# Kernel optimization log

Measured on AMD Instinct MI355X. Metric: run time of the kernel, lower is better.

Reference implementation:

```python
import jax, jax.numpy as jnp
import numpy as np

D_MODEL = 1024
NHEAD = 16
D_K = D_MODEL // NHEAD


def setup_inputs() -> dict:
    key = jax.random.key(0)
    ks = jax.random.split(key, 11)
    B, S = 4, 2048
    s = 1.0 / np.sqrt(D_MODEL)
    return {
        "query": jax.random.normal(ks[0], (B, S, D_MODEL), jnp.float32),
        "key": jax.random.normal(ks[1], (B, S, D_MODEL), jnp.float32),
        "value": jax.random.normal(ks[2], (B, S, D_MODEL), jnp.float32),
        "Wq": jax.random.normal(ks[3], (D_MODEL, D_MODEL), jnp.float32) * s,
        "bq": jnp.zeros((D_MODEL,), jnp.float32),
        "Wk": jax.random.normal(ks[4], (D_MODEL, D_MODEL), jnp.float32) * s,
        "bk": jnp.zeros((D_MODEL,), jnp.float32),
        "Wv": jax.random.normal(ks[5], (D_MODEL, D_MODEL), jnp.float32) * s,
        "bv": jnp.zeros((D_MODEL,), jnp.float32),
        "Wo": jax.random.normal(ks[6], (D_MODEL, D_MODEL), jnp.float32) * s,
        "bo": jnp.zeros((D_MODEL,), jnp.float32),
    }


def _split_heads(x):
    # [B, S, D] -> [B, H, S, d_k]
    B, S, _ = x.shape
    return x.reshape(B, S, NHEAD, D_K).transpose(0, 2, 1, 3)


def reference(query, key, value, Wq, bq, Wk, bk, Wv, bv, Wo, bo):
    # torch Linear: x @ W.T + b
    q = _split_heads(query @ Wq.T + bq)
    k = _split_heads(key @ Wk.T + bk)
    v = _split_heads(value @ Wv.T + bv)
    scale = 1.0 / np.sqrt(D_K).astype(np.float32)
    scores = jnp.einsum("bhqd,bhkd->bhqk", q, k) * scale
    attn = jax.nn.softmax(scores, axis=-1)  # dropout p=0 -> identity
    out = jnp.einsum("bhqk,bhkd->bhqd", attn, v)
    B, H, S, dk = out.shape
    out = out.transpose(0, 2, 1, 3).reshape(B, S, H * dk)
    return out @ Wo.T + bo
```

## Files before the change

kernel.cpp:

```cpp
#include <hip/hip_runtime.h>
#include <stdint.h>

#define DEVI static __device__ __forceinline__

typedef __attribute__((ext_vector_type(4))) float f32x4;
typedef __attribute__((ext_vector_type(16))) float f32x16;
typedef __attribute__((ext_vector_type(8))) __bf16 bf16x8;
typedef __attribute__((ext_vector_type(4))) uint16_t u16x4;
typedef uint16_t u16;

DEVI u16 f2bf(float f) {
  union { float f; uint32_t u; } v; v.f = f;
  uint32_t r = v.u + 0x7FFFu + ((v.u >> 16) & 1u);
  return (u16)(r >> 16);
}

DEVI f32x4 mfma16(bf16x8 a, bf16x8 b, f32x4 c) {
  return __builtin_amdgcn_mfma_f32_16x16x32_bf16(a, b, c, 0, 0, 0);
}

DEVI f32x16 mfma32(bf16x8 a, bf16x8 b, f32x16 c) {
  return __builtin_amdgcn_mfma_f32_32x32x16_bf16(a, b, c, 0, 0, 0);
}

DEVI void load_lds16(const void* g, void* l) {
  __builtin_amdgcn_global_load_lds(
      (const __attribute__((address_space(1))) void*)g,
      (__attribute__((address_space(3))) void*)l, 16, 0, 0);
}

DEVI bf16x8 lds_frag(const u16* p) { return *(const bf16x8*)p; }

DEVI f32x16 zero16() {
  f32x16 z;
#pragma unroll
  for (int i = 0; i < 16; ++i) z[i] = 0.f;
  return z;
}

DEVI float exp2_hw(float x) {
  float r;
  asm("v_exp_f32 %0, %1" : "=v"(r) : "v"(x));
  return r;
}

DEVI uint32_t cvtpk(float lo, float hi) {
  uint32_t r;
  asm("v_cvt_pk_bf16_f32 %0, %1, %2" : "=v"(r) : "v"(lo), "v"(hi));
  return r;
}

DEVI float partner_f(float x) { return __shfl_xor(x, 32, 64); }

DEVI void pswap_asm(uint32_t& a, uint32_t& b) {
  asm("v_permlane32_swap_b32 %0, %1" : "+v"(a), "+v"(b));
}

#define NBIG (4 * 2048 * 1024)
#define NW (1024 * 1024)

__global__ __launch_bounds__(256) void cvt_kernel(
    const float* q, const float* k, const float* v, const float* Wq,
    const float* Wk, const float* Wv, const float* Wo, u16* qb, u16* kb,
    u16* vb, u16* Wqb, u16* Wkb, u16* Wvb, u16* Wob) {
  const float* src;
  u16* dst;
  int n;
  switch (blockIdx.y) {
    case 0: src = q;  dst = qb;  n = NBIG; break;
    case 1: src = k;  dst = kb;  n = NBIG; break;
    case 2: src = v;  dst = vb;  n = NBIG; break;
    case 3: src = Wq; dst = Wqb; n = NW;   break;
    case 4: src = Wk; dst = Wkb; n = NW;   break;
    case 5: src = Wv; dst = Wvb; n = NW;   break;
    default: src = Wo; dst = Wob; n = NW;  break;
  }
  int i = (blockIdx.x * 256 + threadIdx.x) * 4;
  if (i >= n) return;
  float4 f = *(const float4*)&src[i];
  u16x4 o;
  o.x = f2bf(f.x); o.y = f2bf(f.y); o.z = f2bf(f.z); o.w = f2bf(f.w);
  *(u16x4*)&dst[i] = o;
}

DEVI void gemm_core_1024(const u16* __restrict__ A, const u16* __restrict__ Bm,
                         int bm, int bn, u16* As, u16* Bs, f32x4 acc[4][4]) {
  const int tid = threadIdx.x;
  const int w = tid >> 6, l = tid & 63;
  const int lr = l & 15, lg = l >> 4;
  const int wr = (w >> 1) * 64, wc = (w & 1) * 64;

  for (int i = 0; i < 4; ++i)
    for (int j = 0; j < 4; ++j) acc[i][j] = (f32x4){0.f, 0.f, 0.f, 0.f};

  const int c0 = 2 * w, c1 = 2 * w + 1;
  const u16* gA0 = A + (size_t)(bm * 128 + c0 * 16 + (l >> 2)) * 1024 + (l & 3) * 8;
  const u16* gA1 = A + (size_t)(bm * 128 + c1 * 16 + (l >> 2)) * 1024 + (l & 3) * 8;
  const u16* gB0 = Bm + (size_t)(bn * 128 + c0 * 16 + (l >> 2)) * 1024 + (l & 3) * 8;
  const u16* gB1 = Bm + (size_t)(bn * 128 + c1 * 16 + (l >> 2)) * 1024 + (l & 3) * 8;
  u16* lA0 = As + c0 * 512;
  u16* lA1 = As + c1 * 512;
  u16* lB0 = Bs + c0 * 512;
  u16* lB1 = Bs + c1 * 512;

  int aoff[4], boff[4];
#pragma unroll
  for (int mi = 0; mi < 4; ++mi) aoff[mi] = (wr + mi * 16 + lr) * 32 + lg * 8;
#pragma unroll
  for (int nj = 0; nj < 4; ++nj) boff[nj] = (wc + nj * 16 + lr) * 32 + lg * 8;

  for (int k0 = 0; k0 < 1024; k0 += 32) {
    load_lds16(gA0 + k0, lA0);
    load_lds16(gA1 + k0, lA1);
    load_lds16(gB0 + k0, lB0);
    load_lds16(gB1 + k0, lB1);
    __syncthreads();
    bf16x8 af[4], bff[4];
#pragma unroll
    for (int mi = 0; mi < 4; ++mi) af[mi] = lds_frag(&As[aoff[mi]]);
#pragma unroll
    for (int nj = 0; nj < 4; ++nj) bff[nj] = lds_frag(&Bs[boff[nj]]);
#pragma unroll
    for (int mi = 0; mi < 4; ++mi)
#pragma unroll
      for (int nj = 0; nj < 4; ++nj)
        acc[mi][nj] = mfma16(af[mi], bff[nj], acc[mi][nj]);
    __syncthreads();
  }
}

__global__ __launch_bounds__(256) void proj_kernel(
    const u16* qb, const u16* kb, const u16* vb, const u16* Wq, const u16* Wk,
    const u16* Wv, const float* bq, const float* bk, const float* bv, u16* Qp,
    u16* Kp, u16* Vt) {
  __shared__ __align__(16) u16 As[128 * 32];
  __shared__ __align__(16) u16 Bs[128 * 32];
  const int z = blockIdx.z;
  const u16* A = z == 0 ? qb : z == 1 ? kb : vb;
  const u16* W = z == 0 ? Wq : z == 1 ? Wk : Wv;
  const float* bias = z == 0 ? bq : z == 1 ? bk : bv;

  f32x4 acc[4][4];
  gemm_core_1024(A, W, blockIdx.x, blockIdx.y, As, Bs, acc);

  const int tid = threadIdx.x;
  const int w = tid >> 6, l = tid & 63;
  const int lr = l & 15, lg = l >> 4;
  const int wr = (w >> 1) * 64, wc = (w & 1) * 64;
  const int b = (blockIdx.x * 128) >> 11;

#pragma unroll
  for (int nj = 0; nj < 4; ++nj) {
    const int col = blockIdx.y * 128 + wc + nj * 16 + lr;
    const float bb = bias[col];
    const int h = col >> 6, d = col & 63;
#pragma unroll
    for (int mi = 0; mi < 4; ++mi) {
      const int m0 = blockIdx.x * 128 + wr + mi * 16 + lg * 4;
      const int s0 = m0 & 2047;
      if (z < 2) {
        u16* dst = (z == 0) ? Qp : Kp;
#pragma unroll
        for (int r = 0; r < 4; ++r)
          dst[(((size_t)(b * 16 + h) * 2048) + s0 + r) * 64 + d] =
              f2bf(acc[mi][nj][r] + bb);
      } else {
        u16x4 pk;
        pk.x = f2bf(acc[mi][nj][0] + bb);
        pk.y = f2bf(acc[mi][nj][1] + bb);
        pk.z = f2bf(acc[mi][nj][2] + bb);
        pk.w = f2bf(acc[mi][nj][3] + bb);
        *(u16x4*)&Vt[(((size_t)(b * 16 + h) * 64) + d) * 2048 + s0] = pk;
      }
    }
  }
}

__global__ __launch_bounds__(256) void outproj_kernel(const u16* O,
                                                      const u16* Wo,
                                                      const float* bo,
                                                      float* out) {
  __shared__ __align__(16) u16 As[128 * 32];
  __shared__ __align__(16) u16 Bs[128 * 32];
  f32x4 acc[4][4];
  gemm_core_1024(O, Wo, blockIdx.x, blockIdx.y, As, Bs, acc);

  const int tid = threadIdx.x;
  const int w = tid >> 6, l = tid & 63;
  const int lr = l & 15, lg = l >> 4;
  const int wr = (w >> 1) * 64, wc = (w & 1) * 64;
#pragma unroll
  for (int nj = 0; nj < 4; ++nj) {
    const int col = blockIdx.y * 128 + wc + nj * 16 + lr;
    const float bb = bo[col];
#pragma unroll
    for (int mi = 0; mi < 4; ++mi) {
      const int m0 = blockIdx.x * 128 + wr + mi * 16 + lg * 4;
#pragma unroll
      for (int r = 0; r < 4; ++r)
        out[(size_t)(m0 + r) * 1024 + col] = acc[mi][nj][r] + bb;
    }
  }
}

#define LDPK 72
#define NT 32
__global__ __launch_bounds__(256) void attn_kernel(const u16* Qp, const u16* Kp,
                                                   const u16* Vt, u16* Ob) {
  __shared__ __align__(16) u16 Kl[2][64 * LDPK];
  __shared__ __align__(16) u16 Vl[2][64 * LDPK];

  const int tid = threadIdx.x, w = tid >> 6, l = tid & 63;
  const int q = l & 31, hi = l >> 5;
  const int bh = blockIdx.y;
  const int q0 = blockIdx.x * 128 + w * 32;
  const u16* Qh = Qp + (size_t)bh * 2048 * 64;
  const u16* Kh = Kp + (size_t)bh * 2048 * 64;
  const u16* Vh = Vt + (size_t)bh * 64 * 2048;

  const float SC2 = 0.1803368801f;

  bf16x8 qf[4];
#pragma unroll
  for (int ds = 0; ds < 4; ++ds)
    qf[ds] = *(const bf16x8*)&Qh[(size_t)(q0 + q) * 64 + ds * 16 + hi * 8];

  f32x16 o0 = zero16(), o1 = zero16();
  float m = -1.0e30f, ln = 0.f;

  const int r0 = tid >> 3, g0 = tid & 7;
  const int r1 = r0 + 32;

  int koff[2][4], voff[2][4];
#pragma unroll
  for (int kb = 0; kb < 2; ++kb)
#pragma unroll
    for (int ds = 0; ds < 4; ++ds)
      koff[kb][ds] = (kb * 32 + q) * LDPK + ds * 16 + hi * 8;
#pragma unroll
  for (int db = 0; db < 2; ++db)
#pragma unroll
    for (int ks = 0; ks < 4; ++ks)
      voff[db][ks] = (db * 32 + q) * LDPK + ks * 16 + hi * 8;

  bf16x8 kv0 = *(const bf16x8*)&Kh[r0 * 64 + g0 * 8];
  bf16x8 kv1 = *(const bf16x8*)&Kh[r1 * 64 + g0 * 8];
  bf16x8 vv0 = *(const bf16x8*)&Vh[(size_t)r0 * 2048 + g0 * 8];
  bf16x8 vv1 = *(const bf16x8*)&Vh[(size_t)r1 * 2048 + g0 * 8];
  *(bf16x8*)&Kl[0][r0 * LDPK + g0 * 8] = kv0;
  *(bf16x8*)&Kl[0][r1 * LDPK + g0 * 8] = kv1;
  *(bf16x8*)&Vl[0][r0 * LDPK + g0 * 8] = vv0;
  *(bf16x8*)&Vl[0][r1 * LDPK + g0 * 8] = vv1;
  kv0 = *(const bf16x8*)&Kh[4096 + r0 * 64 + g0 * 8];
  kv1 = *(const bf16x8*)&Kh[4096 + r1 * 64 + g0 * 8];
  vv0 = *(const bf16x8*)&Vh[(size_t)r0 * 2048 + 64 + g0 * 8];
  vv1 = *(const bf16x8*)&Vh[(size_t)r1 * 2048 + 64 + g0 * 8];
  const u16* gk0 = Kh + 2 * 4096 + r0 * 64 + g0 * 8;
  const u16* gk1 = Kh + 2 * 4096 + r1 * 64 + g0 * 8;
  const u16* gv0 = Vh + (size_t)r0 * 2048 + 2 * 64 + g0 * 8;
  const u16* gv1 = Vh + (size_t)r1 * 2048 + 2 * 64 + g0 * 8;
  __syncthreads();

  for (int kt = 0; kt < NT; ++kt) {
    const int cur = kt & 1;
    const u16* Kc = Kl[cur];
    const u16* Vc = Vl[cur];

    f32x16 c0 = zero16(), c1 = zero16();
    __builtin_amdgcn_s_setprio(1);
#pragma unroll
    for (int ds = 0; ds < 4; ++ds)
      c0 = mfma32(lds_frag(&Kc[koff[0][ds]]), qf[ds], c0);
#pragma unroll
    for (int ds = 0; ds < 4; ++ds)
      c1 = mfma32(lds_frag(&Kc[koff[1][ds]]), qf[ds], c1);
    __builtin_amdgcn_s_setprio(0);

    float tm[16];
#pragma unroll
    for (int r = 0; r < 16; ++r) tm[r] = fmaxf(c0[r], c1[r]);
#pragma unroll
    for (int s = 8; s > 0; s >>= 1)
#pragma unroll
      for (int r = 0; r < s; ++r) tm[r] = fmaxf(tm[r], tm[r + s]);
    const float mx = fmaxf(tm[0], partner_f(tm[0]));
    if (!__all(mx - m <= 64.0f)) {
      const float mnew = fmaxf(m, mx);
      const float a = exp2_hw((m - mnew) * SC2);
      m = mnew;
#pragma unroll
      for (int r = 0; r < 16; ++r) { o0[r] *= a; o1[r] *= a; }
      ln *= a;
    }
    const float m2 = m * SC2;
    float p0[16], p1[16];
#pragma unroll
    for (int r = 0; r < 16; ++r) {
      p0[r] = exp2_hw(__builtin_fmaf(c0[r], SC2, -m2));
      p1[r] = exp2_hw(__builtin_fmaf(c1[r], SC2, -m2));
    }
    float ts[16];
#pragma unroll
    for (int r = 0; r < 16; ++r) ts[r] = p0[r] + p1[r];
#pragma unroll
    for (int s = 8; s > 0; s >>= 1)
#pragma unroll
      for (int r = 0; r < s; ++r) ts[r] += ts[r + s];
    ln += ts[0] + partner_f(ts[0]);

    if (kt + 1 < NT) {
      u16* Kn = Kl[cur ^ 1];
      u16* Vn = Vl[cur ^ 1];
      *(bf16x8*)&Kn[r0 * LDPK + g0 * 8] = kv0;
      *(bf16x8*)&Kn[r1 * LDPK + g0 * 8] = kv1;
      *(bf16x8*)&Vn[r0 * LDPK + g0 * 8] = vv0;
      *(bf16x8*)&Vn[r1 * LDPK + g0 * 8] = vv1;
    }
    if (kt + 2 < NT) {
      kv0 = *(const bf16x8*)gk0;
      kv1 = *(const bf16x8*)gk1;
      vv0 = *(const bf16x8*)gv0;
      vv1 = *(const bf16x8*)gv1;
      gk0 += 4096; gk1 += 4096; gv0 += 64; gv1 += 64;
    }

    uint32_t wv[16];
#pragma unroll
    for (int i = 0; i < 8; ++i) {
      wv[i]     = cvtpk(p0[2 * i], p0[2 * i + 1]);
      wv[8 + i] = cvtpk(p1[2 * i], p1[2 * i + 1]);
    }
    bf16x8 pa[4];
#pragma unroll
    for (int ks = 0; ks < 4; ++ks) {
      const int base = (ks >> 1) * 8 + 4 * (ks & 1);
      uint32_t x0 = wv[base],     y0 = wv[base + 2];
      uint32_t x1 = wv[base + 1], y1 = wv[base + 3];
      pswap_asm(x0, y0);
      pswap_asm(x1, y1);
      union { uint32_t u[4]; bf16x8 v; } cvt;
      cvt.u[0] = x0; cvt.u[1] = x1; cvt.u[2] = y0; cvt.u[3] = y1;
      pa[ks] = cvt.v;
    }

    __builtin_amdgcn_s_setprio(1);
#pragma unroll
    for (int ks = 0; ks < 4; ++ks)
      o0 = mfma32(lds_frag(&Vc[voff[0][ks]]), pa[ks], o0);
#pragma unroll
    for (int ks = 0; ks < 4; ++ks)
      o1 = mfma32(lds_frag(&Vc[voff[1][ks]]), pa[ks], o1);
    __builtin_amdgcn_s_setprio(0);

    __syncthreads();
  }

  const int b2 = bh >> 4, h = bh & 15;
  const float inv = 1.0f / ln;
  u16* orow = Ob + ((size_t)(b2 * 2048 + q0 + q)) * 1024 + h * 64;
#pragma unroll
  for (int g = 0; g < 4; ++g) {
    u16x4 pk;
    pk.x = f2bf(o0[4 * g + 0] * inv);
    pk.y = f2bf(o0[4 * g + 1] * inv);
    pk.z = f2bf(o0[4 * g + 2] * inv);
    pk.w = f2bf(o0[4 * g + 3] * inv);
    *(u16x4*)&orow[8 * g + 4 * hi] = pk;
  }
#pragma unroll
  for (int g = 0; g < 4; ++g) {
    u16x4 pk;
    pk.x = f2bf(o1[4 * g + 0] * inv);
    pk.y = f2bf(o1[4 * g + 1] * inv);
    pk.z = f2bf(o1[4 * g + 2] * inv);
    pk.w = f2bf(o1[4 * g + 3] * inv);
    *(u16x4*)&orow[32 + 8 * g + 4 * hi] = pk;
  }
}

extern "C" void kernel_launch(void* const* d_in, const int* in_sizes, int n_in,
                              void* d_out, int out_size, void* d_ws,
                              size_t ws_size, hipStream_t stream) {
  const float* q  = (const float*)d_in[0];
  const float* k  = (const float*)d_in[1];
  const float* v  = (const float*)d_in[2];
  const float* Wq = (const float*)d_in[3];
  const float* bq = (const float*)d_in[4];
  const float* Wk = (const float*)d_in[5];
  const float* bk = (const float*)d_in[6];
  const float* Wv = (const float*)d_in[7];
  const float* bv = (const float*)d_in[8];
  const float* Wo = (const float*)d_in[9];
  const float* bo = (const float*)d_in[10];
  float* out = (float*)d_out;

  u16* ws = (u16*)d_ws;
  u16* qb  = ws;
  u16* kb  = qb + NBIG;
  u16* vb  = kb + NBIG;
  u16* Wqb = vb + NBIG;
  u16* Wkb = Wqb + NW;
  u16* Wvb = Wkb + NW;
  u16* Wob = Wvb + NW;
  u16* Qp  = Wob + NW;
  u16* Kp  = Qp + NBIG;
  u16* Vt  = Kp + NBIG;
  u16* O   = qb;

  cvt_kernel<<<dim3(8192, 7, 1), 256, 0, stream>>>(q, k, v, Wq, Wk, Wv, Wo, qb,
                                                   kb, vb, Wqb, Wkb, Wvb, Wob);
  proj_kernel<<<dim3(64, 8, 3), 256, 0, stream>>>(qb, kb, vb, Wqb, Wkb, Wvb,
                                                  bq, bk, bv, Qp, Kp, Vt);
  attn_kernel<<<dim3(16, 64, 1), 256, 0, stream>>>(Qp, Kp, Vt, O);
  outproj_kernel<<<dim3(64, 8, 1), 256, 0, stream>>>(O, Wob, bo, out);
}
```

Before: 235.6 us.

## Fuse fp32-to-bf16 activation conversion into projection GEMM A-tile loads

The separate conversion pass over the query, key and value activations is removed; the projection GEMM now reads fp32 rows directly, converts them to bf16 in registers, and writes them to LDS. The next k-step's A tile is register-prefetched so the conversion overlaps the MFMA work. The attention softmax row-max reduction also switches to v_max3 instructions. The goal is to avoid writing and re-reading about 48 MB of bf16 intermediates, at the cost of double the global A-read bytes per GEMM tile and more registers per thread.

```diff
diff --git a/kernel.cpp b/kernel.cpp
--- a/kernel.cpp
+++ b/kernel.cpp
@@ -50,33 +50,46 @@
   return r;
 }
 
+DEVI float max3f(float a, float b, float c) {
+  float r;
+  asm("v_max3_f32 %0, %1, %2, %3" : "=v"(r) : "v"(a), "v"(b), "v"(c));
+  return r;
+}
+
 DEVI float partner_f(float x) { return __shfl_xor(x, 32, 64); }
 
 DEVI void pswap_asm(uint32_t& a, uint32_t& b) {
   asm("v_permlane32_swap_b32 %0, %1" : "+v"(a), "+v"(b));
 }
 
+DEVI bf16x8 cvt8(float4 lo, float4 hi) {
+  union { uint32_t u[4]; bf16x8 v; } c;
+  c.u[0] = cvtpk(lo.x, lo.y);
+  c.u[1] = cvtpk(lo.z, lo.w);
+  c.u[2] = cvtpk(hi.x, hi.y);
+  c.u[3] = cvtpk(hi.z, hi.w);
+  return c.v;
+}
+
 #define NBIG (4 * 2048 * 1024)
 #define NW (1024 * 1024)
 
-__global__ __launch_bounds__(256) void cvt_kernel(
-    const float* q, const float* k, const float* v, const float* Wq,
-    const float* Wk, const float* Wv, const float* Wo, u16* qb, u16* kb,
-    u16* vb, u16* Wqb, u16* Wkb, u16* Wvb, u16* Wob) {
+__global__ __launch_bounds__(256) void cvt_kernel(const float* Wq,
+                                                  const float* Wk,
+                                                  const float* Wv,
+                                                  const float* Wo, u16* Wqb,
+                                                  u16* Wkb, u16* Wvb,
+                                                  u16* Wob) {
   const float* src;
   u16* dst;
-  int n;
   switch (blockIdx.y) {
-    case 0: src = q;  dst = qb;  n = NBIG; break;
-    case 1: src = k;  dst = kb;  n = NBIG; break;
-    case 2: src = v;  dst = vb;  n = NBIG; break;
-    case 3: src = Wq; dst = Wqb; n = NW;   break;
-    case 4: src = Wk; dst = Wkb; n = NW;   break;
-    case 5: src = Wv; dst = Wvb; n = NW;   break;
-    default: src = Wo; dst = Wob; n = NW;  break;
+    case 0: src = Wq; dst = Wqb; break;
+    case 1: src = Wk; dst = Wkb; break;
+    case 2: src = Wv; dst = Wvb; break;
+    default: src = Wo; dst = Wob; break;
   }
   int i = (blockIdx.x * 256 + threadIdx.x) * 4;
-  if (i >= n) return;
+  if (i >= NW) return;
   float4 f = *(const float4*)&src[i];
   u16x4 o;
   o.x = f2bf(f.x); o.y = f2bf(f.y); o.z = f2bf(f.z); o.w = f2bf(f.w);
@@ -129,19 +142,77 @@
   }
 }
 
+DEVI void gemm_core_f32A(const float* __restrict__ A32,
+                         const u16* __restrict__ Bm, int bm, int bn, u16* As,
+                         u16* Bs, f32x4 acc[4][4]) {
+  const int tid = threadIdx.x;
+  const int w = tid >> 6, l = tid & 63;
+  const int lr = l & 15, lg = l >> 4;
+  const int wr = (w >> 1) * 64, wc = (w & 1) * 64;
+
+  for (int i = 0; i < 4; ++i)
+    for (int j = 0; j < 4; ++j) acc[i][j] = (f32x4){0.f, 0.f, 0.f, 0.f};
+
+  const int c0 = 2 * w, c1 = 2 * w + 1;
+  const float* gA0 = A32 + (size_t)(bm * 128 + c0 * 16 + (l >> 2)) * 1024 + (l & 3) * 8;
+  const float* gA1 = A32 + (size_t)(bm * 128 + c1 * 16 + (l >> 2)) * 1024 + (l & 3) * 8;
+  const u16* gB0 = Bm + (size_t)(bn * 128 + c0 * 16 + (l >> 2)) * 1024 + (l & 3) * 8;
+  const u16* gB1 = Bm + (size_t)(bn * 128 + c1 * 16 + (l >> 2)) * 1024 + (l & 3) * 8;
+  u16* wA0 = As + c0 * 512 + l * 8;
+  u16* wA1 = As + c1 * 512 + l * 8;
+  u16* lB0 = Bs + c0 * 512;
+  u16* lB1 = Bs + c1 * 512;
+
+  int aoff[4], boff[4];
+#pragma unroll
+  for (int mi = 0; mi < 4; ++mi) aoff[mi] = (wr + mi * 16 + lr) * 32 + lg * 8;
+#pragma unroll
+  for (int nj = 0; nj < 4; ++nj) boff[nj] = (wc + nj * 16 + lr) * 32 + lg * 8;
+
+  float4 a0l = *(const float4*)(gA0);
+  float4 a0h = *(const float4*)(gA0 + 4);
+  float4 a1l = *(const float4*)(gA1);
+  float4 a1h = *(const float4*)(gA1 + 4);
+
+  for (int k0 = 0; k0 < 1024; k0 += 32) {
+    *(bf16x8*)wA0 = cvt8(a0l, a0h);
+    *(bf16x8*)wA1 = cvt8(a1l, a1h);
+    load_lds16(gB0 + k0, lB0);
+    load_lds16(gB1 + k0, lB1);
+    __syncthreads();
+    if (k0 + 32 < 1024) {
+      a0l = *(const float4*)(gA0 + k0 + 32);
+      a0h = *(const float4*)(gA0 + k0 + 36);
+      a1l = *(const float4*)(gA1 + k0 + 32);
+      a1h = *(const float4*)(gA1 + k0 + 36);
+    }
+    bf16x8 af[4], bff[4];
+#pragma unroll
+    for (int mi = 0; mi < 4; ++mi) af[mi] = lds_frag(&As[aoff[mi]]);
+#pragma unroll
+    for (int nj = 0; nj < 4; ++nj) bff[nj] = lds_frag(&Bs[boff[nj]]);
+#pragma unroll
+    for (int mi = 0; mi < 4; ++mi)
+#pragma unroll
+      for (int nj = 0; nj < 4; ++nj)
+        acc[mi][nj] = mfma16(af[mi], bff[nj], acc[mi][nj]);
+    __syncthreads();
+  }
+}
+
 __global__ __launch_bounds__(256) void proj_kernel(
-    const u16* qb, const u16* kb, const u16* vb, const u16* Wq, const u16* Wk,
-    const u16* Wv, const float* bq, const float* bk, const float* bv, u16* Qp,
-    u16* Kp, u16* Vt) {
+    const float* qx, const float* kx, const float* vx, const u16* Wq,
+    const u16* Wk, const u16* Wv, const float* bq, const float* bk,
+    const float* bv, u16* Qp, u16* Kp, u16* Vt) {
   __shared__ __align__(16) u16 As[128 * 32];
   __shared__ __align__(16) u16 Bs[128 * 32];
   const int z = blockIdx.z;
-  const u16* A = z == 0 ? qb : z == 1 ? kb : vb;
+  const float* A = z == 0 ? qx : z == 1 ? kx : vx;
   const u16* W = z == 0 ? Wq : z == 1 ? Wk : Wv;
   const float* bias = z == 0 ? bq : z == 1 ? bk : bv;
 
   f32x4 acc[4][4];
-  gemm_core_1024(A, W, blockIdx.x, blockIdx.y, As, Bs, acc);
+  gemm_core_f32A(A, W, blockIdx.x, blockIdx.y, As, Bs, acc);
 
   const int tid = threadIdx.x;
   const int w = tid >> 6, l = tid & 63;
@@ -279,10 +350,16 @@
     float tm[16];
 #pragma unroll
     for (int r = 0; r < 16; ++r) tm[r] = fmaxf(c0[r], c1[r]);
-#pragma unroll
-    for (int s = 8; s > 0; s >>= 1)
-#pragma unroll
-      for (int r = 0; r < s; ++r) tm[r] = fmaxf(tm[r], tm[r + s]);
+    {
+      const float m0_ = max3f(tm[0], tm[1], tm[2]);
+      const float m1_ = max3f(tm[3], tm[4], tm[5]);
+      const float m2_ = max3f(tm[6], tm[7], tm[8]);
+      const float m3_ = max3f(tm[9], tm[10], tm[11]);
+      const float m4_ = max3f(tm[12], tm[13], tm[14]);
+      const float a_ = max3f(m0_, m1_, m2_);
+      const float b_ = max3f(m3_, m4_, tm[15]);
+      tm[0] = fmaxf(a_, b_);
+    }
     const float mx = fmaxf(tm[0], partner_f(tm[0]));
     if (!__all(mx - m <= 64.0f)) {
       const float mnew = fmaxf(m, mx);
@@ -395,22 +472,19 @@
   float* out = (float*)d_out;
 
   u16* ws = (u16*)d_ws;
-  u16* qb  = ws;
-  u16* kb  = qb + NBIG;
-  u16* vb  = kb + NBIG;
-  u16* Wqb = vb + NBIG;
+  u16* Wqb = ws;
   u16* Wkb = Wqb + NW;
   u16* Wvb = Wkb + NW;
   u16* Wob = Wvb + NW;
   u16* Qp  = Wob + NW;
   u16* Kp  = Qp + NBIG;
   u16* Vt  = Kp + NBIG;
-  u16* O   = qb;
-
-  cvt_kernel<<<dim3(8192, 7, 1), 256, 0, stream>>>(q, k, v, Wq, Wk, Wv, Wo, qb,
-                                                   kb, vb, Wqb, Wkb, Wvb, Wob);
-  proj_kernel<<<dim3(64, 8, 3), 256, 0, stream>>>(qb, kb, vb, Wqb, Wkb, Wvb,
-                                                  bq, bk, bv, Qp, Kp, Vt);
+  u16* O   = Vt + NBIG;
+
+  cvt_kernel<<<dim3(1024, 4, 1), 256, 0, stream>>>(Wq, Wk, Wv, Wo, Wqb, Wkb,
+                                                   Wvb, Wob);
+  proj_kernel<<<dim3(64, 8, 3), 256, 0, stream>>>(q, k, v, Wqb, Wkb, Wvb, bq,
+                                                  bk, bv, Qp, Kp, Vt);
   attn_kernel<<<dim3(16, 64, 1), 256, 0, stream>>>(Qp, Kp, Vt, O);
   outproj_kernel<<<dim3(64, 8, 1), 256, 0, stream>>>(O, Wob, bo, out);
 }
```

Result: slower. 245.7 us (+4.3%).

## Use 512-thread attention blocks sharing K/V tiles; reduce max with v_max3

Applied to the files above, without the earlier changes.

The attention kernel now runs 8 waves per block, covering 256 queries instead of 128, and launches half as many blocks. Each K/V tile staged in LDS is therefore reused by twice as many waves, and each thread loads one row instead of two. The row-max reduction is rewritten with v_max3_f32 to cut VALU instructions. In exchange the grid shrinks to 512 blocks, which may lower occupancy flexibility and adds register pressure under the 512-thread launch bound.

```diff
diff --git a/kernel.cpp b/kernel.cpp
--- a/kernel.cpp
+++ b/kernel.cpp
@@ -47,6 +47,12 @@
 DEVI uint32_t cvtpk(float lo, float hi) {
   uint32_t r;
   asm("v_cvt_pk_bf16_f32 %0, %1, %2" : "=v"(r) : "v"(lo), "v"(hi));
+  return r;
+}
+
+DEVI float max3f(float a, float b, float c) {
+  float r;
+  asm("v_max3_f32 %0, %1, %2, %3" : "=v"(r) : "v"(a), "v"(b), "v"(c));
   return r;
 }
 
@@ -205,7 +211,7 @@
 
 #define LDPK 72
 #define NT 32
-__global__ __launch_bounds__(256) void attn_kernel(const u16* Qp, const u16* Kp,
+__global__ __launch_bounds__(512) void attn_kernel(const u16* Qp, const u16* Kp,
                                                    const u16* Vt, u16* Ob) {
   __shared__ __align__(16) u16 Kl[2][64 * LDPK];
   __shared__ __align__(16) u16 Vl[2][64 * LDPK];
@@ -213,7 +219,7 @@
   const int tid = threadIdx.x, w = tid >> 6, l = tid & 63;
   const int q = l & 31, hi = l >> 5;
   const int bh = blockIdx.y;
-  const int q0 = blockIdx.x * 128 + w * 32;
+  const int q0 = blockIdx.x * 256 + w * 32;
   const u16* Qh = Qp + (size_t)bh * 2048 * 64;
   const u16* Kh = Kp + (size_t)bh * 2048 * 64;
   const u16* Vh = Vt + (size_t)bh * 64 * 2048;
@@ -228,8 +234,7 @@
   f32x16 o0 = zero16(), o1 = zero16();
   float m = -1.0e30f, ln = 0.f;
 
-  const int r0 = tid >> 3, g0 = tid & 7;
-  const int r1 = r0 + 32;
+  const int srow = tid >> 3, g0 = tid & 7;
 
   int koff[2][4], voff[2][4];
 #pragma unroll
@@ -243,22 +248,14 @@
     for (int ks = 0; ks < 4; ++ks)
       voff[db][ks] = (db * 32 + q) * LDPK + ks * 16 + hi * 8;
 
-  bf16x8 kv0 = *(const bf16x8*)&Kh[r0 * 64 + g0 * 8];
-  bf16x8 kv1 = *(const bf16x8*)&Kh[r1 * 64 + g0 * 8];
-  bf16x8 vv0 = *(const bf16x8*)&Vh[(size_t)r0 * 2048 + g0 * 8];
-  bf16x8 vv1 = *(const bf16x8*)&Vh[(size_t)r1 * 2048 + g0 * 8];
-  *(bf16x8*)&Kl[0][r0 * LDPK + g0 * 8] = kv0;
-  *(bf16x8*)&Kl[0][r1 * LDPK + g0 * 8] = kv1;
-  *(bf16x8*)&Vl[0][r0 * LDPK + g0 * 8] = vv0;
-  *(bf16x8*)&Vl[0][r1 * LDPK + g0 * 8] = vv1;
-  kv0 = *(const bf16x8*)&Kh[4096 + r0 * 64 + g0 * 8];
-  kv1 = *(const bf16x8*)&Kh[4096 + r1 * 64 + g0 * 8];
-  vv0 = *(const bf16x8*)&Vh[(size_t)r0 * 2048 + 64 + g0 * 8];
-  vv1 = *(const bf16x8*)&Vh[(size_t)r1 * 2048 + 64 + g0 * 8];
-  const u16* gk0 = Kh + 2 * 4096 + r0 * 64 + g0 * 8;
-  const u16* gk1 = Kh + 2 * 4096 + r1 * 64 + g0 * 8;
-  const u16* gv0 = Vh + (size_t)r0 * 2048 + 2 * 64 + g0 * 8;
-  const u16* gv1 = Vh + (size_t)r1 * 2048 + 2 * 64 + g0 * 8;
+  bf16x8 kv = *(const bf16x8*)&Kh[srow * 64 + g0 * 8];
+  bf16x8 vv = *(const bf16x8*)&Vh[(size_t)srow * 2048 + g0 * 8];
+  *(bf16x8*)&Kl[0][srow * LDPK + g0 * 8] = kv;
+  *(bf16x8*)&Vl[0][srow * LDPK + g0 * 8] = vv;
+  kv = *(const bf16x8*)&Kh[4096 + srow * 64 + g0 * 8];
+  vv = *(const bf16x8*)&Vh[(size_t)srow * 2048 + 64 + g0 * 8];
+  const u16* gk = Kh + 2 * 4096 + srow * 64 + g0 * 8;
+  const u16* gv = Vh + (size_t)srow * 2048 + 2 * 64 + g0 * 8;
   __syncthreads();
 
   for (int kt = 0; kt < NT; ++kt) {
@@ -279,10 +276,16 @@
     float tm[16];
 #pragma unroll
     for (int r = 0; r < 16; ++r) tm[r] = fmaxf(c0[r], c1[r]);
-#pragma unroll
-    for (int s = 8; s > 0; s >>= 1)
-#pragma unroll
-      for (int r = 0; r < s; ++r) tm[r] = fmaxf(tm[r], tm[r + s]);
+    {
+      const float m0_ = max3f(tm[0], tm[1], tm[2]);
+      const float m1_ = max3f(tm[3], tm[4], tm[5]);
+      const float m2_ = max3f(tm[6], tm[7], tm[8]);
+      const float m3_ = max3f(tm[9], tm[10], tm[11]);
+      const float m4_ = max3f(tm[12], tm[13], tm[14]);
+      const float a_ = max3f(m0_, m1_, m2_);
+      const float b_ = max3f(m3_, m4_, tm[15]);
+      tm[0] = fmaxf(a_, b_);
+    }
     const float mx = fmaxf(tm[0], partner_f(tm[0]));
     if (!__all(mx - m <= 64.0f)) {
       const float mnew = fmaxf(m, mx);
@@ -309,19 +312,13 @@
     ln += ts[0] + partner_f(ts[0]);
 
     if (kt + 1 < NT) {
-      u16* Kn = Kl[cur ^ 1];
-      u16* Vn = Vl[cur ^ 1];
-      *(bf16x8*)&Kn[r0 * LDPK + g0 * 8] = kv0;
-      *(bf16x8*)&Kn[r1 * LDPK + g0 * 8] = kv1;
-      *(bf16x8*)&Vn[r0 * LDPK + g0 * 8] = vv0;
-      *(bf16x8*)&Vn[r1 * LDPK + g0 * 8] = vv1;
+      *(bf16x8*)&Kl[cur ^ 1][srow * LDPK + g0 * 8] = kv;
+      *(bf16x8*)&Vl[cur ^ 1][srow * LDPK + g0 * 8] = vv;
     }
     if (kt + 2 < NT) {
-      kv0 = *(const bf16x8*)gk0;
-      kv1 = *(const bf16x8*)gk1;
-      vv0 = *(const bf16x8*)gv0;
-      vv1 = *(const bf16x8*)gv1;
-      gk0 += 4096; gk1 += 4096; gv0 += 64; gv1 += 64;
+      kv = *(const bf16x8*)gk;
+      vv = *(const bf16x8*)gv;
+      gk += 4096; gv += 64;
     }
 
     uint32_t wv[16];
@@ -411,6 +408,6 @@
                                                    kb, vb, Wqb, Wkb, Wvb, Wob);
   proj_kernel<<<dim3(64, 8, 3), 256, 0, stream>>>(qb, kb, vb, Wqb, Wkb, Wvb,
                                                   bq, bk, bv, Qp, Kp, Vt);
-  attn_kernel<<<dim3(16, 64, 1), 256, 0, stream>>>(Qp, Kp, Vt, O);
+  attn_kernel<<<dim3(8, 64, 1), 512, 0, stream>>>(Qp, Kp, Vt, O);
   outproj_kernel<<<dim3(64, 8, 1), 256, 0, stream>>>(O, Wob, bo, out);
 }
```

Result: faster. 230.3 us (-2.3%).
